# Performance work log

Measured on AMD Instinct MI355X. Metric: run time of the kernel, lower is better.

## Reference

```python
import jax, jax.numpy as jnp
import numpy as np

E, B, S, D, F = 8, 2, 1024, 1024, 4096


def setup_inputs() -> dict:
    key = jax.random.key(0)
    ks = jax.random.split(key, 9)
    sc_d = 1.0 / np.sqrt(D)
    sc_f = 1.0 / np.sqrt(F)
    hidden_states = jax.random.normal(ks[0], (B, S, D), dtype=jnp.float32)
    # router outputs set externally on the parent model in the original code
    gating_probs = jax.nn.softmax(jax.random.normal(ks[1], (B, E), dtype=jnp.float32), axis=-1)
    shared_gate_prob = jax.nn.sigmoid(jax.random.normal(ks[2], (B, 1), dtype=jnp.float32))
    # stacked expert SwiGLU MLP weights (Llama-style gate/up/down)
    Wg = jax.random.normal(ks[3], (E, D, F), dtype=jnp.float32) * sc_d
    Wu = jax.random.normal(ks[4], (E, D, F), dtype=jnp.float32) * sc_d
    Wd = jax.random.normal(ks[5], (E, F, D), dtype=jnp.float32) * sc_f
    # shared expert MLP
    Sg = jax.random.normal(ks[6], (D, F), dtype=jnp.float32) * sc_d
    Su = jax.random.normal(ks[7], (D, F), dtype=jnp.float32) * sc_d
    Sd = jax.random.normal(ks[8], (F, D), dtype=jnp.float32) * sc_f
    return {
        "hidden_states": hidden_states,
        "gating_probs": gating_probs,
        "shared_gate_prob": shared_gate_prob,
        "Wg": Wg, "Wu": Wu, "Wd": Wd,
        "Sg": Sg, "Su": Su, "Sd": Sd,
    }


def reference(hidden_states, gating_probs, shared_gate_prob, Wg, Wu, Wd, Sg, Su, Sd):
    h = hidden_states  # [B,S,D]
    # every expert's MLP runs on all tokens (naive all-experts-dense, as in source)
    g = jnp.einsum("bsd,edf->ebsf", h, Wg)
    u = jnp.einsum("bsd,edf->ebsf", h, Wu)
    expert_outs = jnp.einsum("ebsf,efd->ebsd", jax.nn.silu(g) * u, Wd)  # [E,B,S,D]
    # weighted_sum routing with per-sequence gating probs [B,E]
    expert_output = jnp.einsum("be,ebsd->bsd", gating_probs, expert_outs)
    # shared expert MLP
    shared = jnp.einsum("bsf,fd->bsd", jax.nn.silu(h @ Sg) * (h @ Su), Sd)
    sg = shared_gate_prob[:, :, None]  # [B,1,1]
    return (1.0 - sg) * expert_output + sg * shared
```

## Files before the change

kernel.cpp:

```cpp
#include <hip/hip_runtime.h>
#include <cstdio>
#include <cstdint>

typedef _Float16 f16;
typedef _Float16 f16x4 __attribute__((ext_vector_type(4)));
typedef _Float16 f16x8 __attribute__((ext_vector_type(8)));
typedef float f32x4 __attribute__((ext_vector_type(4)));

#define GLL16(gp, lp)                                                          \
  __builtin_amdgcn_global_load_lds(                                            \
      (const __attribute__((address_space(1))) void*)(gp),                     \
      (__attribute__((address_space(3))) void*)(lp), 16, 0, 0)

#define BARX __builtin_amdgcn_s_barrier()
#define WAITV8 { asm volatile("s_waitcnt vmcnt(8)" ::: "memory"); __builtin_amdgcn_sched_barrier(0); }
#define WAITV4 { asm volatile("s_waitcnt vmcnt(4)" ::: "memory"); __builtin_amdgcn_sched_barrier(0); }
#define WAITV0 { asm volatile("s_waitcnt vmcnt(0)" ::: "memory"); __builtin_amdgcn_sched_barrier(0); }
#define WAITL0 { asm volatile("s_waitcnt lgkmcnt(0)" ::: "memory"); __builtin_amdgcn_sched_barrier(0); }

__global__ void cvt_f32_f16_kernel(const float* __restrict__ in,
                                   f16* __restrict__ out, int n4) {
  int i = blockIdx.x * blockDim.x + threadIdx.x;
  if (i < n4) {
    f32x4 v = reinterpret_cast<const f32x4*>(in)[i];
    f16x4 o;
    o[0] = (f16)v[0]; o[1] = (f16)v[1]; o[2] = (f16)v[2]; o[3] = (f16)v[3];
    reinterpret_cast<f16x4*>(out)[i] = o;
  }
}

__global__ void tr_cvt2_kernel(const float* __restrict__ inA,
                               const float* __restrict__ inB,
                               f16* __restrict__ out, size_t slotOff,
                               int C, size_t OS, int nA) {
  int slot = blockIdx.z;
  const float* src = (slot < nA) ? inA + (size_t)slot * 64 * gridDim.y * C : inB;
  f16* dst = out + (size_t)slot * slotOff;
  __shared__ f16 tl[4096];
  int t = threadIdx.x;
  int r0 = blockIdx.y * 64, c0 = blockIdx.x * 64;
  int br = (t >> 4) * 4, bc = (t & 15) * 4;
  f32x4 v[4];
#pragma unroll
  for (int i = 0; i < 4; ++i)
    v[i] = *(const f32x4*)&src[(size_t)(r0 + br + i) * C + c0 + bc];
#pragma unroll
  for (int cc = 0; cc < 4; ++cc) {
    int c = bc + cc;
    f16x4 o;
    o[0] = (f16)v[0][cc]; o[1] = (f16)v[1][cc];
    o[2] = (f16)v[2][cc]; o[3] = (f16)v[3][cc];
    *(f16x4*)&tl[c * 64 + (br ^ ((c & 7) * 8))] = o;
  }
  __syncthreads();
  int rw = (t & 7) * 8, cw = t >> 3;
#pragma unroll
  for (int j = 0; j < 2; ++j) {
    int c = cw + j * 32;
    f16x8 o = *(const f16x8*)&tl[c * 64 + (rw ^ ((c & 7) * 8))];
    *(f16x8*)&dst[(size_t)(c0 + c) * OS + r0 + rw] = o;
  }
}

#define STAGE_T(NB, TILE)                                                      \
  do {                                                                         \
    const f16* a_ = aS + (size_t)(TILE) * 64;                                  \
    f16* da_ = &lds[(NB) * 16384 + ldsT];                                      \
    GLL16(a_, da_); GLL16(a_ + 65536, da_ + 4096);                             \
    GLL16(a_ + 131072, da_ + 8192); GLL16(a_ + 196608, da_ + 12288);           \
    const f16* g_ = gS + (size_t)(TILE) * 64;                                  \
    f16* dg_ = &lds[32768 + (NB) * 16384 + ldsT];                              \
    GLL16(g_, dg_); GLL16(g_ + 65536, dg_ + 4096);                             \
    const f16* u_ = uS + (size_t)(TILE) * 64;                                  \
    GLL16(u_, dg_ + 8192); GLL16(u_ + 65536, dg_ + 12288);                     \
  } while (0)

#define RD3(BUF, VK)                                                           \
  do {                                                                         \
    const f16* pa_ = &lds[(BUF) * 16384 + wr * 4096 + vRow + (VK)];            \
    aF[0] = *(const f16x8*)(pa_);                                              \
    aF[1] = *(const f16x8*)(pa_ + 1024);                                       \
    aF[2] = *(const f16x8*)(pa_ + 2048);                                       \
    aF[3] = *(const f16x8*)(pa_ + 3072);                                       \
    const f16* pg_ = &lds[32768 + (BUF) * 16384 + wc * 4096 + vRow + (VK)];    \
    bG[0] = *(const f16x8*)(pg_);                                              \
    bG[1] = *(const f16x8*)(pg_ + 1024);                                       \
    bG[2] = *(const f16x8*)(pg_ + 2048);                                       \
    bG[3] = *(const f16x8*)(pg_ + 3072);                                       \
    const f16* pu_ = pg_ + 8192;                                               \
    bU[0] = *(const f16x8*)(pu_);                                              \
    bU[1] = *(const f16x8*)(pu_ + 1024);                                       \
    bU[2] = *(const f16x8*)(pu_ + 2048);                                       \
    bU[3] = *(const f16x8*)(pu_ + 3072);                                       \
  } while (0)

#define MFMA32()                                                               \
  do {                                                                         \
    __builtin_amdgcn_s_setprio(1);                                             \
    _Pragma("unroll") for (int mi = 0; mi < 4; ++mi)                           \
        _Pragma("unroll") for (int ni = 0; ni < 4; ++ni) {                     \
      ag[mi][ni] = __builtin_amdgcn_mfma_f32_16x16x32_f16(aF[mi], bG[ni],      \
                                                          ag[mi][ni], 0, 0, 0);\
      au[mi][ni] = __builtin_amdgcn_mfma_f32_16x16x32_f16(aF[mi], bU[ni],      \
                                                          au[mi][ni], 0, 0, 0);\
    }                                                                          \
    __builtin_amdgcn_s_setprio(0);                                             \
    __builtin_amdgcn_sched_barrier(0);                                         \
  } while (0)

#define BODY4(BUF, TILE, DOST, WV)                                             \
  do {                                                                         \
    RD3(BUF, vK0);                                                             \
    WAITL0;                                                                    \
    MFMA32();                                                                  \
    RD3(BUF, vK1);                                                             \
    WAITL0;                                                                    \
    BARX;                                                                      \
    if (DOST) { STAGE_T(BUF, TILE); }                                          \
    MFMA32();                                                                  \
    WV;                                                                        \
    BARX;                                                                      \
  } while (0)

__global__ __launch_bounds__(512, 2) void gemmUG3_kernel(
    const f16* __restrict__ A, const f16* __restrict__ Bg,
    const f16* __restrict__ Bu, f16* __restrict__ T,
    const float* __restrict__ gate, const float* __restrict__ sgp) {
  __shared__ __align__(16) f16 lds[65536];

  int lgl = (blockIdx.x & 7) * 288 + (blockIdx.x >> 3);
  int mt = lgl & 7;
  int ntg = lgl >> 3;
  int slot = ntg >> 5;

  int t = threadIdx.x, w = t >> 6, l = t & 63;
  int wr = w >> 1, wc = w & 1;

  int kqs = (((t & 7) ^ ((t >> 3) & 7)) * 8);
  const f16* aS = A + (size_t)(mt * 256 + (t >> 3)) * 1024 + kqs;
  const f16* gS = Bg + (size_t)slot * 4194304 +
                  (size_t)((ntg & 31) * 128 + (t >> 3)) * 1024 + kqs;
  const f16* uS = Bu + (size_t)slot * 4194304 +
                  (size_t)((ntg & 31) * 128 + (t >> 3)) * 1024 + kqs;
  int ldsT = t * 8;

  int vRow = (l & 15) * 64;
  int vK0 = (((l >> 4) ^ (l & 7))) * 8;
  int vK1 = (((4 + (l >> 4)) ^ (l & 7))) * 8;

  f16x8 aF[4], bG[4], bU[4];
  f32x4 ag[4][4] = {}, au[4][4] = {};

  STAGE_T(0, 0);
  STAGE_T(1, 1);
  WAITV8; BARX;

#pragma unroll 1
  for (int it = 0; it < 7; ++it) {
    BODY4(0, 2 * it + 2, 1, WAITV8);
    BODY4(1, 2 * it + 3, 1, WAITV8);
  }
  BODY4(0, 0, 0, WAITV0);
  BODY4(1, 0, 0, {});

  int r0 = (l >> 4) * 4, c0 = l & 15;
  int rowb = mt * 256 + wr * 64;
  size_t colb = (size_t)ntg * 128 + wc * 64;
  int b = mt >> 2;
  float s = sgp[b];
  float coef = (slot < 8) ? (1.f - s) * gate[b * 8 + slot] : s;
#pragma unroll
  for (int mi = 0; mi < 4; ++mi) {
#pragma unroll
    for (int ni = 0; ni < 4; ++ni) {
#pragma unroll
      for (int j = 0; j < 4; ++j) {
        float g = ag[mi][ni][j];
        float u = au[mi][ni][j];
        T[(size_t)(rowb + mi * 16 + r0 + j) * 36864 + colb + ni * 16 + c0] =
            (f16)(g / (1.f + __expf(-g)) * u * coef);
      }
    }
  }
}

#define STAGE_A(tile, hf)                                                      \
  do {                                                                         \
    const f16* g_ = Abase + (size_t)((hf) * 128) * LD + (tile) * 64 + aVoff;   \
    f16* d_ = &lds[(2 * ((tile) & 1) + (hf)) * 8192 + w * 512];                \
    GLL16(g_, d_);                                                             \
    GLL16(g_ + (size_t)64 * LD, d_ + 4096);                                    \
  } while (0)
#define STAGE_B(tile, hf)                                                      \
  do {                                                                         \
    const f16* g_ = Bbase + (size_t)((hf) * 128) * LD + (tile) * 64 + aVoff;   \
    f16* d_ = &lds[32768 + (2 * ((tile) & 1) + (hf)) * 8192 + w * 512];        \
    GLL16(g_, d_);                                                             \
    GLL16(g_ + (size_t)64 * LD, d_ + 4096);                                    \
  } while (0)

#define RD_A(rh, buf)                                                          \
  do {                                                                         \
    const f16* p_ = &lds[(2 * (buf) + wr) * 8192 + (rh) * 4096];               \
    aFd[0][0] = *(const f16x8*)(p_ + 0 * 1024 + vR0);                          \
    aFd[0][1] = *(const f16x8*)(p_ + 0 * 1024 + vR1);                          \
    aFd[1][0] = *(const f16x8*)(p_ + 1 * 1024 + vR0);                          \
    aFd[1][1] = *(const f16x8*)(p_ + 1 * 1024 + vR1);                          \
    aFd[2][0] = *(const f16x8*)(p_ + 2 * 1024 + vR0);                          \
    aFd[2][1] = *(const f16x8*)(p_ + 2 * 1024 + vR1);                          \
    aFd[3][0] = *(const f16x8*)(p_ + 3 * 1024 + vR0);                          \
    aFd[3][1] = *(const f16x8*)(p_ + 3 * 1024 + vR1);                          \
  } while (0)
#define RD_B(ch, buf)                                                          \
  do {                                                                         \
    const f16* p_ = &lds[32768 + (2 * (buf) + bh) * 8192 + bq * 4096 +         \
                         (ch) * 2 * 1024];                                     \
    bFd[(ch) * 2][0] = *(const f16x8*)(p_ + vR0);                              \
    bFd[(ch) * 2][1] = *(const f16x8*)(p_ + vR1);                              \
    bFd[(ch) * 2 + 1][0] = *(const f16x8*)(p_ + 1024 + vR0);                   \
    bFd[(ch) * 2 + 1][1] = *(const f16x8*)(p_ + 1024 + vR1);                   \
  } while (0)

#define MFMA16(rh, ch)                                                         \
  do {                                                                         \
    __builtin_amdgcn_s_setprio(1);                                             \
    _Pragma("unroll") for (int rt = 0; rt < 4; ++rt)                           \
        _Pragma("unroll") for (int ct = 0; ct < 2; ++ct)                       \
        _Pragma("unroll") for (int ks = 0; ks < 2; ++ks)                       \
            acc[(rh) * 4 + rt][(ch) * 2 + ct] =                                \
        __builtin_amdgcn_mfma_f32_16x16x32_f16(                                \
            aFd[rt][ks], bFd[(ch) * 2 + ct][ks],                               \
            acc[(rh) * 4 + rt][(ch) * 2 + ct], 0, 0, 0);                       \
    __builtin_amdgcn_s_setprio(0);                                             \
    __builtin_amdgcn_sched_barrier(0);                                         \
  } while (0)

__global__ __launch_bounds__(512, 2) void gemmD_kernel(
    const f16* __restrict__ A, const f16* __restrict__ B,
    float* __restrict__ P) {
  constexpr size_t LD = 36864;
  constexpr int NTILES = 72;
  __shared__ __align__(16) f16 lds[65536];

  int wg = (blockIdx.x & 7) * 32 + (blockIdx.x >> 3);
  int kpart = wg >> 5, mt = (wg >> 2) & 7, nt = wg & 3;

  int t = threadIdx.x, w = t >> 6, l = t & 63;
  int wr = w >> 2, wc = w & 3;
  int bh = wc >> 1, bq = wc & 1;

  int scol = (((l & 7) ^ ((l >> 3) & 7)) * 8);
  size_t stRow = (size_t)(w * 8 + (l >> 3)) * LD;
  size_t aVoff = stRow + scol;
  const f16* Abase = A + (size_t)mt * 256 * LD + (size_t)kpart * 4608;
  const f16* Bbase = B + (size_t)nt * 256 * LD + (size_t)kpart * 4608;

  int vR0 = (l & 15) * 64 + (((l >> 4) * 8) ^ ((l & 7) * 8));
  int vR1 = (l & 15) * 64 + ((32 + (l >> 4) * 8) ^ ((l & 7) * 8));

  f16x8 aFd[4][2], bFd[4][2];
  f32x4 acc[8][4] = {};

  STAGE_B(0, 0); STAGE_B(0, 1);
  STAGE_A(0, 0); STAGE_A(0, 1);
  STAGE_B(1, 0); STAGE_B(1, 1);
  WAITV4;
  BARX;

#pragma unroll 1
  for (int it = 0; it < NTILES / 2 - 1; ++it) {
    int t1 = 2 * it + 1, t2 = 2 * it + 2, t3 = 2 * it + 3;
    RD_A(0, 0); RD_B(0, 0); STAGE_A(t1, 0);
    BARX; WAITL0; MFMA16(0, 0); BARX;
    RD_B(1, 0); STAGE_A(t1, 1);
    BARX; WAITL0; MFMA16(0, 1); BARX;
    RD_A(1, 0); STAGE_B(t2, 0);
    BARX; WAITL0; MFMA16(1, 0); BARX;
    STAGE_B(t2, 1);
    BARX; MFMA16(1, 1); WAITV4; BARX;
    RD_A(0, 1); RD_B(0, 1); STAGE_A(t2, 0);
    BARX; WAITL0; MFMA16(0, 0); BARX;
    RD_B(1, 1); STAGE_A(t2, 1);
    BARX; WAITL0; MFMA16(0, 1); BARX;
    RD_A(1, 1); STAGE_B(t3, 0);
    BARX; WAITL0; MFMA16(1, 0); BARX;
    STAGE_B(t3, 1);
    BARX; MFMA16(1, 1); WAITV4; BARX;
  }
  RD_A(0, 0); RD_B(0, 0); STAGE_A(NTILES - 1, 0);
  BARX; WAITL0; MFMA16(0, 0); BARX;
  RD_B(1, 0); STAGE_A(NTILES - 1, 1);
  BARX; WAITL0; MFMA16(0, 1); BARX;
  RD_A(1, 0);
  BARX; WAITL0; MFMA16(1, 0); BARX;
  BARX; MFMA16(1, 1); WAITV0; BARX;
  RD_A(0, 1); RD_B(0, 1);
  BARX; WAITL0; MFMA16(0, 0); BARX;
  RD_B(1, 1);
  BARX; WAITL0; MFMA16(0, 1); BARX;
  RD_A(1, 1);
  BARX; WAITL0; MFMA16(1, 0); BARX;
  MFMA16(1, 1);

  int r0 = (l >> 4) * 4, c0 = l & 15;
  size_t base = ((size_t)kpart << 21);
  int rowbase = mt * 256 + wr * 128;
  int colbase = nt * 256 + wc * 64;
#pragma unroll
  for (int rt = 0; rt < 8; ++rt)
#pragma unroll
    for (int ct = 0; ct < 4; ++ct)
#pragma unroll
      for (int j = 0; j < 4; ++j)
        P[base + (size_t)(rowbase + rt * 16 + r0 + j) * 1024 + colbase +
          ct * 16 + c0] = acc[rt][ct][j];
}

__global__ void reduce8_kernel(const float* __restrict__ P,
                               float* __restrict__ out, int n4) {
  int i = blockIdx.x * blockDim.x + threadIdx.x;
  if (i < n4) {
    f32x4 s = {0.f, 0.f, 0.f, 0.f};
#pragma unroll
    for (int e = 0; e < 8; ++e) {
      f32x4 v = reinterpret_cast<const f32x4*>(P + ((size_t)e << 21))[i];
      s += v;
    }
    reinterpret_cast<f32x4*>(out)[i] = s;
  }
}

extern "C" void kernel_launch(void* const* d_in, const int* in_sizes, int n_in,
                              void* d_out, int out_size, void* d_ws,
                              size_t ws_size, hipStream_t stream) {
  const float* h    = (const float*)d_in[0];
  const float* gate = (const float*)d_in[1];
  const float* sgp  = (const float*)d_in[2];
  const float* Wg   = (const float*)d_in[3];
  const float* Wu   = (const float*)d_in[4];
  const float* Wd   = (const float*)d_in[5];
  const float* Sg   = (const float*)d_in[6];
  const float* Su   = (const float*)d_in[7];
  const float* Sd   = (const float*)d_in[8];

  const size_t SZ_HB = 4194304;
  const size_t SZ_W  = 75497472;
  const size_t SZ_T  = 150994944;
  const size_t SZ_P  = 67108864;
  char* ws = (char*)d_ws;
  f16*   hb  = (f16*)(ws);
  f16*   WgT = (f16*)(ws + SZ_HB);
  f16*   WuT = (f16*)(ws + SZ_HB + SZ_W);
  f16*   WdT = (f16*)(ws + SZ_HB + 2 * SZ_W);
  f16*   T   = (f16*)(ws + SZ_HB + 3 * SZ_W);
  float* P   = (float*)(ws + SZ_HB + 3 * SZ_W + SZ_T);
  size_t need = SZ_HB + 3 * SZ_W + SZ_T + SZ_P;
  if (ws_size < need) {
    fprintf(stderr, "kernel_launch: ws too small (%zu < %zu)\n", ws_size, need);
    return;
  }
  float* out = (float*)d_out;

  cvt_f32_f16_kernel<<<2048, 256, 0, stream>>>(h, hb, 524288);
  tr_cvt2_kernel<<<dim3(64, 16, 9), 256, 0, stream>>>(
      Wg, Sg, WgT, 4096ull * 1024, 4096, 1024, 8);
  tr_cvt2_kernel<<<dim3(64, 16, 9), 256, 0, stream>>>(
      Wu, Su, WuT, 4096ull * 1024, 4096, 1024, 8);
  tr_cvt2_kernel<<<dim3(16, 64, 9), 256, 0, stream>>>(
      Wd, Sd, WdT, 4096, 1024, 36864, 8);

  gemmUG3_kernel<<<2304, 512, 0, stream>>>(hb, WgT, WuT, T, gate, sgp);
  gemmD_kernel<<<256, 512, 0, stream>>>(T, WdT, P);
  reduce8_kernel<<<2048, 256, 0, stream>>>(P, out, 524288);
}
```

Baseline: 564.8 us.

## Restructure gate/up GEMM into 4-stage K=32 pipeline with 2x4 warp grid

Rewrites the fused gate/up GEMM so each K step is 32 wide and staged through a 4-deep LDS ring buffer instead of a 2-deep K=64 double buffer. The warp layout changes from 4x2 to 2x4, so each warp owns 128 rows by 32 columns and reuses the A fragments across G/U. Loads are split into A and G/U halves interleaved with the MFMA groups, with a new swizzle for the narrower tiles. The aim is deeper prefetch and better latency hiding. The cost is more barriers per unit of K and a different LDS read pattern that may cause bank conflicts.

Result: slower. 582.7 us (+3.2%).

```diff
diff --git a/kernel.cpp b/kernel.cpp
--- a/kernel.cpp
+++ b/kernel.cpp
@@ -62,67 +62,65 @@
   }
 }
 
-#define STAGE_T(NB, TILE)                                                      \
-  do {                                                                         \
-    const f16* a_ = aS + (size_t)(TILE) * 64;                                  \
-    f16* da_ = &lds[(NB) * 16384 + ldsT];                                      \
-    GLL16(a_, da_); GLL16(a_ + 65536, da_ + 4096);                             \
-    GLL16(a_ + 131072, da_ + 8192); GLL16(a_ + 196608, da_ + 12288);           \
-    const f16* g_ = gS + (size_t)(TILE) * 64;                                  \
-    f16* dg_ = &lds[32768 + (NB) * 16384 + ldsT];                              \
-    GLL16(g_, dg_); GLL16(g_ + 65536, dg_ + 4096);                             \
-    const f16* u_ = uS + (size_t)(TILE) * 64;                                  \
-    GLL16(u_, dg_ + 8192); GLL16(u_ + 65536, dg_ + 12288);                     \
-  } while (0)
-
-#define RD3(BUF, VK)                                                           \
-  do {                                                                         \
-    const f16* pa_ = &lds[(BUF) * 16384 + wr * 4096 + vRow + (VK)];            \
+#define STG_A4(B)                                                              \
+  {                                                                            \
+    GLL16(aS, &lds[(B) * 16384 + dA]);                                         \
+    GLL16(aS + 131072, &lds[(B) * 16384 + 4096 + dA]);                         \
+  }
+#define STG_GU4(B)                                                             \
+  {                                                                            \
+    GLL16(gS, &lds[(B) * 16384 + 8192 + dA]);                                  \
+    GLL16(uS, &lds[(B) * 16384 + 12288 + dA]);                                 \
+    aS += 32; gS += 32; uS += 32;                                              \
+  }
+
+#define RD_G1(B)                                                               \
+  do {                                                                         \
+    const f16* pa_ = &lds[(B) * 16384 + voffA];                                \
     aF[0] = *(const f16x8*)(pa_);                                              \
-    aF[1] = *(const f16x8*)(pa_ + 1024);                                       \
-    aF[2] = *(const f16x8*)(pa_ + 2048);                                       \
-    aF[3] = *(const f16x8*)(pa_ + 3072);                                       \
-    const f16* pg_ = &lds[32768 + (BUF) * 16384 + wc * 4096 + vRow + (VK)];    \
-    bG[0] = *(const f16x8*)(pg_);                                              \
-    bG[1] = *(const f16x8*)(pg_ + 1024);                                       \
-    bG[2] = *(const f16x8*)(pg_ + 2048);                                       \
-    bG[3] = *(const f16x8*)(pg_ + 3072);                                       \
-    const f16* pu_ = pg_ + 8192;                                               \
-    bU[0] = *(const f16x8*)(pu_);                                              \
-    bU[1] = *(const f16x8*)(pu_ + 1024);                                       \
-    bU[2] = *(const f16x8*)(pu_ + 2048);                                       \
-    bU[3] = *(const f16x8*)(pu_ + 3072);                                       \
-  } while (0)
-
-#define MFMA32()                                                               \
+    aF[1] = *(const f16x8*)(pa_ + 512);                                        \
+    aF[2] = *(const f16x8*)(pa_ + 1024);                                       \
+    aF[3] = *(const f16x8*)(pa_ + 1536);                                       \
+    const f16* pb_ = &lds[(B) * 16384 + voffB];                                \
+    bG[0] = *(const f16x8*)(pb_);                                              \
+    bG[1] = *(const f16x8*)(pb_ + 512);                                        \
+    bU[0] = *(const f16x8*)(pb_ + 4096);                                       \
+    bU[1] = *(const f16x8*)(pb_ + 4608);                                       \
+  } while (0)
+#define RD_G2(B)                                                               \
+  do {                                                                         \
+    const f16* pa_ = &lds[(B) * 16384 + voffA + 2048];                         \
+    aF[0] = *(const f16x8*)(pa_);                                              \
+    aF[1] = *(const f16x8*)(pa_ + 512);                                        \
+    aF[2] = *(const f16x8*)(pa_ + 1024);                                       \
+    aF[3] = *(const f16x8*)(pa_ + 1536);                                       \
+  } while (0)
+
+#define MFMAG(G)                                                               \
   do {                                                                         \
     __builtin_amdgcn_s_setprio(1);                                             \
     _Pragma("unroll") for (int mi = 0; mi < 4; ++mi)                           \
-        _Pragma("unroll") for (int ni = 0; ni < 4; ++ni) {                     \
-      ag[mi][ni] = __builtin_amdgcn_mfma_f32_16x16x32_f16(aF[mi], bG[ni],      \
-                                                          ag[mi][ni], 0, 0, 0);\
-      au[mi][ni] = __builtin_amdgcn_mfma_f32_16x16x32_f16(aF[mi], bU[ni],      \
-                                                          au[mi][ni], 0, 0, 0);\
+        _Pragma("unroll") for (int ni = 0; ni < 2; ++ni) {                     \
+      ag[(G) * 4 + mi][ni] = __builtin_amdgcn_mfma_f32_16x16x32_f16(           \
+          aF[mi], bG[ni], ag[(G) * 4 + mi][ni], 0, 0, 0);                      \
+      au[(G) * 4 + mi][ni] = __builtin_amdgcn_mfma_f32_16x16x32_f16(           \
+          aF[mi], bU[ni], au[(G) * 4 + mi][ni], 0, 0, 0);                      \
     }                                                                          \
     __builtin_amdgcn_s_setprio(0);                                             \
     __builtin_amdgcn_sched_barrier(0);                                         \
   } while (0)
 
-#define BODY4(BUF, TILE, DOST, WV)                                             \
-  do {                                                                         \
-    RD3(BUF, vK0);                                                             \
-    WAITL0;                                                                    \
-    MFMA32();                                                                  \
-    RD3(BUF, vK1);                                                             \
-    WAITL0;                                                                    \
-    BARX;                                                                      \
-    if (DOST) { STAGE_T(BUF, TILE); }                                          \
-    MFMA32();                                                                  \
-    WV;                                                                        \
-    BARX;                                                                      \
-  } while (0)
-
-__global__ __launch_bounds__(512, 2) void gemmUG3_kernel(
+#define KT4(B, DOST, WV)                                                       \
+  do {                                                                         \
+    RD_G1(B);                                                                  \
+    if (DOST) STG_A4(((B) + 3) & 3);                                           \
+    BARX; WAITL0; MFMAG(0); BARX;                                              \
+    RD_G2(B);                                                                  \
+    if (DOST) STG_GU4(((B) + 3) & 3);                                          \
+    BARX; WAITL0; MFMAG(1); WV; BARX;                                          \
+  } while (0)
+
+__global__ __launch_bounds__(512, 2) void gemmUG4_kernel(
     const f16* __restrict__ A, const f16* __restrict__ Bg,
     const f16* __restrict__ Bu, f16* __restrict__ T,
     const float* __restrict__ gate, const float* __restrict__ sgp) {
@@ -132,52 +130,60 @@
   int mt = lgl & 7;
   int ntg = lgl >> 3;
   int slot = ntg >> 5;
+  int ntl = ntg & 31;
 
   int t = threadIdx.x, w = t >> 6, l = t & 63;
-  int wr = w >> 1, wc = w & 1;
-
-  int kqs = (((t & 7) ^ ((t >> 3) & 7)) * 8);
-  const f16* aS = A + (size_t)(mt * 256 + (t >> 3)) * 1024 + kqs;
+  int wr = w >> 2, wc = w & 3;
+
+  int arow = t >> 2;
+  int aswz = ((t & 3) ^ ((arow >> 1) & 3)) * 8;
+  const f16* aS = A + (size_t)(mt * 256 + arow) * 1024 + aswz;
   const f16* gS = Bg + (size_t)slot * 4194304 +
-                  (size_t)((ntg & 31) * 128 + (t >> 3)) * 1024 + kqs;
+                  (size_t)(ntl * 128 + arow) * 1024 + aswz;
   const f16* uS = Bu + (size_t)slot * 4194304 +
-                  (size_t)((ntg & 31) * 128 + (t >> 3)) * 1024 + kqs;
-  int ldsT = t * 8;
-
-  int vRow = (l & 15) * 64;
-  int vK0 = (((l >> 4) ^ (l & 7))) * 8;
-  int vK1 = (((4 + (l >> 4)) ^ (l & 7))) * 8;
-
-  f16x8 aF[4], bG[4], bU[4];
-  f32x4 ag[4][4] = {}, au[4][4] = {};
-
-  STAGE_T(0, 0);
-  STAGE_T(1, 1);
+                  (size_t)(ntl * 128 + arow) * 1024 + aswz;
+  int dA = t * 8;
+
+  int r15 = l & 15;
+  int swz = ((l >> 4) ^ ((r15 >> 1) & 3)) * 8;
+  int voffA = wr * 4096 + r15 * 32 + swz;
+  int voffB = 8192 + wc * 1024 + r15 * 32 + swz;
+
+  f16x8 aF[4], bG[2], bU[2];
+  f32x4 ag[8][2] = {}, au[8][2] = {};
+
+  STG_A4(0); STG_GU4(0);
+  STG_A4(1); STG_GU4(1);
+  STG_A4(2); STG_GU4(2);
   WAITV8; BARX;
 
 #pragma unroll 1
   for (int it = 0; it < 7; ++it) {
-    BODY4(0, 2 * it + 2, 1, WAITV8);
-    BODY4(1, 2 * it + 3, 1, WAITV8);
-  }
-  BODY4(0, 0, 0, WAITV0);
-  BODY4(1, 0, 0, {});
+    KT4(0, 1, WAITV8);
+    KT4(1, 1, WAITV8);
+    KT4(2, 1, WAITV8);
+    KT4(3, 1, WAITV8);
+  }
+  KT4(0, 1, WAITV8);
+  KT4(1, 0, WAITV4);
+  KT4(2, 0, WAITV0);
+  KT4(3, 0, {});
 
   int r0 = (l >> 4) * 4, c0 = l & 15;
-  int rowb = mt * 256 + wr * 64;
-  size_t colb = (size_t)ntg * 128 + wc * 64;
+  int rowb = mt * 256 + wr * 128;
+  size_t colb = (size_t)ntg * 128 + wc * 32;
   int b = mt >> 2;
   float s = sgp[b];
   float coef = (slot < 8) ? (1.f - s) * gate[b * 8 + slot] : s;
 #pragma unroll
-  for (int mi = 0; mi < 4; ++mi) {
-#pragma unroll
-    for (int ni = 0; ni < 4; ++ni) {
+  for (int rt = 0; rt < 8; ++rt) {
+#pragma unroll
+    for (int ni = 0; ni < 2; ++ni) {
 #pragma unroll
       for (int j = 0; j < 4; ++j) {
-        float g = ag[mi][ni][j];
-        float u = au[mi][ni][j];
-        T[(size_t)(rowb + mi * 16 + r0 + j) * 36864 + colb + ni * 16 + c0] =
+        float g = ag[rt][ni][j];
+        float u = au[rt][ni][j];
+        T[(size_t)(rowb + rt * 16 + r0 + j) * 36864 + colb + ni * 16 + c0] =
             (f16)(g / (1.f + __expf(-g)) * u * coef);
       }
     }
@@ -369,7 +375,7 @@
   tr_cvt2_kernel<<<dim3(16, 64, 9), 256, 0, stream>>>(
       Wd, Sd, WdT, 4096, 1024, 36864, 8);
 
-  gemmUG3_kernel<<<2304, 512, 0, stream>>>(hb, WgT, WuT, T, gate, sgp);
+  gemmUG4_kernel<<<2304, 512, 0, stream>>>(hb, WgT, WuT, T, gate, sgp);
   gemmD_kernel<<<256, 512, 0, stream>>>(T, WdT, P);
   reduce8_kernel<<<2048, 256, 0, stream>>>(P, out, 524288);
 }
```
